# Optimization experiments

Hardware: AMD Instinct MI355X
Metric: run time of the kernel (lower is better)

Reference implementation:

```python
import jax, jax.numpy as jnp
import numpy as np
import math

B, N, D, H = 4, 2048, 1024, 16
HD = D // H  # head dim = 64


def setup_inputs() -> dict:
    key = jax.random.key(0)
    ks = jax.random.split(key, 5)
    x = jax.random.normal(ks[0], (B, N, D), dtype=jnp.float32)
    # per-head kqv Linear: weight (3*HD, D), bias (3*HD), stacked over heads
    Wkqv = jax.random.normal(ks[1], (H, 3 * HD, D), dtype=jnp.float32) / math.sqrt(D)
    bkqv = jax.random.normal(ks[2], (H, 3 * HD), dtype=jnp.float32) * 0.02
    # output projection Linear(D, D)
    Wproj = jax.random.normal(ks[3], (D, D), dtype=jnp.float32) / math.sqrt(D)
    bproj = jax.random.normal(ks[4], (D,), dtype=jnp.float32) * 0.02
    return {"x": x, "Wkqv": Wkqv, "bkqv": bkqv, "Wproj": Wproj, "bproj": bproj}


def reference(x, Wkqv, bkqv, Wproj, bproj):
    # per-head linear: y = x @ W.T + b  -> [B, H, N, 3*HD]
    kqv = jnp.einsum('bnd,hed->bhne', x, Wkqv) + bkqv[None, :, None, :]
    k, q, v = jnp.split(kqv, 3, axis=-1)  # each [B, H, N, HD]
    # scores = q @ k^T / sqrt(HD)   (attention_scores(k, q) -> q @ k.T)
    scores = jnp.einsum('bhqd,bhkd->bhqk', q, k) / math.sqrt(HD)
    causal = jnp.tril(jnp.ones((N, N), dtype=bool))
    scores = jnp.where(causal[None, None], scores, -jnp.inf)
    att = jax.nn.softmax(scores, axis=-1)
    out = jnp.einsum('bhqk,bhkd->bhqd', att, v)  # [B, H, N, HD]
    # concat heads: [B, N, H*HD]
    sa = out.transpose(0, 2, 1, 3).reshape(B, N, D)
    # dropout is identity in eval mode; final projection
    return sa @ Wproj.T + bproj
```

## Files before the change

kernel.cpp:

```cpp
#include <hip/hip_runtime.h>
#include <hip/hip_bf16.h>


#define NSEQ 2048
#define NHEAD 16
#define DMODEL 1024
#define SCALE2 0.18033688011112042f

typedef __attribute__((ext_vector_type(8))) short v8s;
typedef __attribute__((ext_vector_type(4))) float v4f;

__device__ __forceinline__ float bf2f(unsigned short u) {
    union { unsigned int i; float f; } v;
    v.i = ((unsigned int)u) << 16;
    return v.f;
}
__device__ __forceinline__ unsigned short f2bf(float f) {
    unsigned int x = __float_as_uint(f);
    return (unsigned short)((x + 0x7fffu + ((x >> 16) & 1u)) >> 16);
}
__device__ __forceinline__ unsigned short f2bf_rh(float f) {
    return (unsigned short)((__float_as_uint(f) + 0x8000u) >> 16);
}
__device__ __forceinline__ float fast_exp2(float x) {
#if __has_builtin(__builtin_amdgcn_exp2f)
    return __builtin_amdgcn_exp2f(x);
#else
    return __expf(x * 0.69314718056f);
#endif
}
__device__ __forceinline__ void gld_lds16(const unsigned short* g, unsigned short* l) {
    __builtin_amdgcn_global_load_lds(
        (const __attribute__((address_space(1))) void*)g,
        (__attribute__((address_space(3))) void*)l, 16, 0, 0);
}

__global__ __launch_bounds__(256) void cvt_bf16(
    const float* __restrict__ x, const float* __restrict__ wk, const float* __restrict__ wp,
    unsigned short* __restrict__ xb, unsigned short* __restrict__ wkb,
    unsigned short* __restrict__ wpb)
{
    const int i = blockIdx.x * 256 + threadIdx.x;
    const float* s; unsigned short* d; int o;
    if (i < 2097152)      { s = x;  d = xb;  o = i; }
    else if (i < 2883584) {
        s = wk; d = wkb;
        const int oi  = i - 2097152;
        const int row = oi >> 8, cq = oi & 255;
        const int h   = row / 192;
        const int rem = row - h * 192;
        const int cls = rem >> 6, e = rem & 63;
        float4 f = ((const float4*)s)[oi];
        ushort4 u;
        u.x = f2bf(f.x); u.y = f2bf(f.y); u.z = f2bf(f.z); u.w = f2bf(f.w);
        ((ushort4*)d)[(((cls << 10) + (h << 6) + e) << 8) + cq] = u;
        return;
    }
    else                  { s = wp; d = wpb; o = i - 2883584; }
    float4 f = ((const float4*)s)[o];
    ushort4 u;
    u.x = f2bf(f.x); u.y = f2bf(f.y); u.z = f2bf(f.z); u.w = f2bf(f.w);
    ((ushort4*)d)[o] = u;
}

template <int EPI>
__global__ __launch_bounds__(256, 3) void gemm_lds(
    const unsigned short* __restrict__ A, const unsigned short* __restrict__ B,
    const float* __restrict__ bias,
    float* __restrict__ Cf,
    unsigned short* __restrict__ Kb, unsigned short* __restrict__ Qb,
    unsigned short* __restrict__ VTb,
    int M, int Nc, int K)
{
    __shared__ __align__(16) unsigned short Al[3][4096];
    __shared__ __align__(16) unsigned short Bl[3][4096];

    const int t = threadIdx.x, wave = t >> 6, lane = t & 63;
    const int wm = wave >> 1, wn = wave & 1;

    const int lin = blockIdx.y * gridDim.x + blockIdx.x;
    const int xcd = lin & 7, pos = lin >> 3;
    const int by  = (xcd << 3) + (pos & 7);
    const int bx  = pos >> 3;
    const int m0 = by * 128, n0 = bx * 128;
    const int quad = lane >> 4, c = lane & 15;

    const int g0 = wave * 2, g1 = wave * 2 + 1;
    const int r15 = lane & 15, kg = (lane >> 4) & 3;
    const unsigned short* sA0 = A + (size_t)(m0 + g0 * 16 + r15) * K + kg * 8;
    const unsigned short* sA1 = A + (size_t)(m0 + g1 * 16 + r15) * K + kg * 8;
    const unsigned short* sB0 = B + (size_t)(n0 + g0 * 16 + r15) * K + kg * 8;
    const unsigned short* sB1 = B + (size_t)(n0 + g1 * 16 + r15) * K + kg * 8;

    v4f acc[4][4];
#pragma unroll
    for (int i = 0; i < 4; ++i)
#pragma unroll
        for (int j = 0; j < 4; ++j) acc[i][j] = (v4f){0.f, 0.f, 0.f, 0.f};

    const int fbase = (quad * 16 + c) * 8;
    const int nt = K >> 5;

    auto stage = [&](int b, int tt) {
        const int o = tt << 5;
        unsigned short* la = &Al[b][0];
        unsigned short* lb = &Bl[b][0];
        gld_lds16(sA0 + o, la + g0 * 512);
        gld_lds16(sA1 + o, la + g1 * 512);
        gld_lds16(sB0 + o, lb + g0 * 512);
        gld_lds16(sB1 + o, lb + g1 * 512);
    };

    stage(0, 0);
    stage(1, 1);
    asm volatile("s_waitcnt vmcnt(4)" ::: "memory");
    __builtin_amdgcn_s_barrier();

    int cur = 0;
    for (int tt = 0; tt < nt; ++tt) {
        const int nxt = (cur == 2) ? 0 : cur + 1;
        const int b2  = (nxt == 2) ? 0 : nxt + 1;
        const bool pf = (tt + 2 < nt);
        if (pf) stage(b2, tt + 2);

        v8s af[4], bfr[4];
#pragma unroll
        for (int ms = 0; ms < 4; ++ms)
            af[ms] = *(const v8s*)&Al[cur][(wm * 4 + ms) * 512 + fbase];
#pragma unroll
        for (int ns = 0; ns < 4; ++ns)
            bfr[ns] = *(const v8s*)&Bl[cur][(wn * 4 + ns) * 512 + fbase];
#pragma unroll
        for (int ms = 0; ms < 4; ++ms)
#pragma unroll
            for (int ns = 0; ns < 4; ++ns)
                acc[ms][ns] = __builtin_amdgcn_mfma_f32_16x16x32_bf16(
                    af[ms], bfr[ns], acc[ms][ns], 0, 0, 0);

        if (pf) { asm volatile("s_waitcnt vmcnt(4)" ::: "memory"); }
        else    { asm volatile("s_waitcnt vmcnt(0)" ::: "memory"); }
        __builtin_amdgcn_s_barrier();
        cur = nxt;
    }

#pragma unroll
    for (int ms = 0; ms < 4; ++ms) {
        const int row0 = m0 + wm * 64 + ms * 16 + quad * 4;
#pragma unroll
        for (int ns = 0; ns < 4; ++ns) {
            const int colbase = n0 + wn * 64 + ns * 16;
            float bn, scl = 1.f;
            if (EPI == 2) {
                bn = bias[colbase + c];
            } else {
                const int cls = colbase >> 10;
                const int wi  = colbase & 1023;
                const int h   = wi >> 6, e0 = wi & 63;
                bn = bias[h * 192 + cls * 64 + e0 + c];
                if (cls == 1) scl = SCALE2;
            }
            float v0 = (acc[ms][ns][0] + bn) * scl;
            float v1 = (acc[ms][ns][1] + bn) * scl;
            float v2 = (acc[ms][ns][2] + bn) * scl;
            float v3 = (acc[ms][ns][3] + bn) * scl;
            if (EPI == 2) {
                float* pc = Cf + (size_t)row0 * Nc + colbase + c;
                pc[0] = v0; pc[(size_t)Nc] = v1;
                pc[(size_t)2 * Nc] = v2; pc[(size_t)3 * Nc] = v3;
            } else {
                const int cls = colbase >> 10;
                const int wi  = colbase & 1023;
                const int h   = wi >> 6, e = (wi & 63) + c;
                const int bb  = row0 >> 11, tok0 = row0 & 2047;
                const int bhh = bb * 16 + h;
                if (cls == 2) {
                    ushort4 pk;
                    pk.x = f2bf(v0); pk.y = f2bf(v1); pk.z = f2bf(v2); pk.w = f2bf(v3);
                    *(ushort4*)(VTb + ((size_t)bhh * 64 + e) * 2048 + tok0) = pk;
                } else {
                    unsigned short* dst = (cls == 0) ? Kb : Qb;
                    const size_t base = ((size_t)bhh * 2048 + tok0) * 64 + e;
                    dst[base]       = f2bf(v0);
                    dst[base + 64]  = f2bf(v1);
                    dst[base + 128] = f2bf(v2);
                    dst[base + 192] = f2bf(v3);
                }
            }
        }
    }
}

template <bool A_BF16, int EPI>
__global__ __launch_bounds__(256) void gemm_mfma(
    const void* __restrict__ Av, const float* __restrict__ B,
    const float* __restrict__ bias,
    float* __restrict__ Cf,
    unsigned short* __restrict__ Kb, unsigned short* __restrict__ Qb,
    unsigned short* __restrict__ VTb,
    int M, int Nc, int K)
{
    __shared__ __align__(16) unsigned short Al[512 * 8];
    __shared__ __align__(16) unsigned short Bl[512 * 8];

    const int t = threadIdx.x;
    const int wave = t >> 6, lane = t & 63;
    const int wm = wave >> 1, wn = wave & 1;
    const int m0 = blockIdx.y * 128, n0 = blockIdx.x * 128;
    const int quad = lane >> 4, c = lane & 15;

    const int srow = t >> 1, skh = t & 1;
    const int sslot = (srow >> 4) * 64 + (skh * 2) * 16 + (srow & 15);

    v4f acc[4][4];
#pragma unroll
    for (int i = 0; i < 4; ++i)
#pragma unroll
        for (int j = 0; j < 4; ++j) acc[i][j] = (v4f){0.f, 0.f, 0.f, 0.f};

    const unsigned short* pa_u = (const unsigned short*)Av + (size_t)(m0 + srow) * K + skh * 16;
    const float*          pa_f = (const float*)Av          + (size_t)(m0 + srow) * K + skh * 16;
    const float*          pb   = B                          + (size_t)(n0 + srow) * K + skh * 16;

    const int fbase = (quad * 16 + c) * 8;

    for (int k0 = 0; k0 < K; k0 += 32) {
        unsigned short a16[16], b16[16];
        if (A_BF16) {
            uint4 r0 = *(const uint4*)(pa_u + k0);
            uint4 r1 = *(const uint4*)(pa_u + k0 + 8);
            *(uint4*)&a16[0] = r0; *(uint4*)&a16[8] = r1;
        } else {
            float4 f0 = *(const float4*)(pa_f + k0);
            float4 f1 = *(const float4*)(pa_f + k0 + 4);
            float4 f2 = *(const float4*)(pa_f + k0 + 8);
            float4 f3 = *(const float4*)(pa_f + k0 + 12);
            a16[0] = f2bf_rh(f0.x); a16[1] = f2bf_rh(f0.y); a16[2] = f2bf_rh(f0.z); a16[3] = f2bf_rh(f0.w);
            a16[4] = f2bf_rh(f1.x); a16[5] = f2bf_rh(f1.y); a16[6] = f2bf_rh(f1.z); a16[7] = f2bf_rh(f1.w);
            a16[8] = f2bf_rh(f2.x); a16[9] = f2bf_rh(f2.y); a16[10] = f2bf_rh(f2.z); a16[11] = f2bf_rh(f2.w);
            a16[12] = f2bf_rh(f3.x); a16[13] = f2bf_rh(f3.y); a16[14] = f2bf_rh(f3.z); a16[15] = f2bf_rh(f3.w);
        }
        {
            float4 g0 = *(const float4*)(pb + k0);
            float4 g1 = *(const float4*)(pb + k0 + 4);
            float4 g2 = *(const float4*)(pb + k0 + 8);
            float4 g3 = *(const float4*)(pb + k0 + 12);
            b16[0] = f2bf_rh(g0.x); b16[1] = f2bf_rh(g0.y); b16[2] = f2bf_rh(g0.z); b16[3] = f2bf_rh(g0.w);
            b16[4] = f2bf_rh(g1.x); b16[5] = f2bf_rh(g1.y); b16[6] = f2bf_rh(g1.z); b16[7] = f2bf_rh(g1.w);
            b16[8] = f2bf_rh(g2.x); b16[9] = f2bf_rh(g2.y); b16[10] = f2bf_rh(g2.z); b16[11] = f2bf_rh(g2.w);
            b16[12] = f2bf_rh(g3.x); b16[13] = f2bf_rh(g3.y); b16[14] = f2bf_rh(g3.z); b16[15] = f2bf_rh(g3.w);
        }
        __syncthreads();
        *(uint4*)&Al[sslot * 8]        = *(uint4*)&a16[0];
        *(uint4*)&Al[(sslot + 16) * 8] = *(uint4*)&a16[8];
        *(uint4*)&Bl[sslot * 8]        = *(uint4*)&b16[0];
        *(uint4*)&Bl[(sslot + 16) * 8] = *(uint4*)&b16[8];
        __syncthreads();

        v8s af[4], bf[4];
#pragma unroll
        for (int ms = 0; ms < 4; ++ms)
            af[ms] = *(const v8s*)&Al[(wm * 4 + ms) * 512 + fbase];
#pragma unroll
        for (int ns = 0; ns < 4; ++ns)
            bf[ns] = *(const v8s*)&Bl[(wn * 4 + ns) * 512 + fbase];
#pragma unroll
        for (int ms = 0; ms < 4; ++ms)
#pragma unroll
            for (int ns = 0; ns < 4; ++ns)
                acc[ms][ns] = __builtin_amdgcn_mfma_f32_16x16x32_bf16(
                    af[ms], bf[ns], acc[ms][ns], 0, 0, 0);
    }

#pragma unroll
    for (int ms = 0; ms < 4; ++ms) {
        const int row0 = m0 + wm * 64 + ms * 16 + quad * 4;
#pragma unroll
        for (int ns = 0; ns < 4; ++ns) {
            const int colbase = n0 + wn * 64 + ns * 16;
            float bn = (EPI == 2) ? bias[colbase + c] : bias[colbase + c];
            float v0 = acc[ms][ns][0] + bn;
            float v1 = acc[ms][ns][1] + bn;
            float v2 = acc[ms][ns][2] + bn;
            float v3 = acc[ms][ns][3] + bn;
            if (EPI == 2) {
                float* pc = Cf + (size_t)row0 * Nc + colbase + c;
                pc[0] = v0; pc[(size_t)Nc] = v1;
                pc[(size_t)2 * Nc] = v2; pc[(size_t)3 * Nc] = v3;
            } else {
                const int hh = colbase / 192;
                const int eb = colbase - hh * 192;
                const int bb = row0 >> 11, tok0 = row0 & 2047;
                const int bhh = bb * 16 + hh;
                if (eb >= 128) {
                    ushort4 pk;
                    pk.x = f2bf(v0); pk.y = f2bf(v1); pk.z = f2bf(v2); pk.w = f2bf(v3);
                    *(ushort4*)(VTb + ((size_t)bhh * 64 + (eb - 128) + c) * 2048 + tok0) = pk;
                } else {
                    const bool isq = (eb >= 64);
                    const float s = isq ? SCALE2 : 1.f;
                    unsigned short* dst = isq ? Qb : Kb;
                    const int e = (isq ? eb - 64 : eb) + c;
                    const size_t base = ((size_t)bhh * 2048 + tok0) * 64 + e;
                    dst[base]       = f2bf(v0 * s);
                    dst[base + 64]  = f2bf(v1 * s);
                    dst[base + 128] = f2bf(v2 * s);
                    dst[base + 192] = f2bf(v3 * s);
                }
            }
        }
    }
}

#define ATTS 72

__global__ __launch_bounds__(256, 2) void attn_mfma(
    const unsigned short* __restrict__ Kbuf,
    const unsigned short* __restrict__ Qbuf,
    const unsigned short* __restrict__ VT,
    unsigned short* __restrict__ sa)
{
    __shared__ __align__(16) unsigned short Ps[4][64 * ATTS];

    const int t = threadIdx.x, w = t >> 6, lane = t & 63;
    const int quad = lane >> 4, c = lane & 15;
    const int bh = blockIdx.x & 63, bq = blockIdx.x >> 6;
    const int b = bh >> 4, hh = bh & 15;
    const int qt = (w == 0) ? bq : (w == 1) ? (15 - bq) : (w == 2) ? (16 + bq) : (31 - bq);
    const int qw = qt * 64;
    const size_t gbase = (size_t)bh * (2048 * 64);

    const int rs  = c & 3;
    const int rc0 = (quad ^ rs) * 8, rc1 = 32 + rc0;
    unsigned short* PsW = &Ps[w][0];

    v8s qf[4][2];
#pragma unroll
    for (int qs = 0; qs < 4; ++qs) {
        const unsigned short* qp = Qbuf + gbase + (size_t)(qw + qs * 16 + c) * 64 + quad * 8;
        qf[qs][0] = *(const v8s*)qp;
        qf[qs][1] = *(const v8s*)(qp + 32);
    }
    v4f oacc[4][4], lacc[4];
#pragma unroll
    for (int qs = 0; qs < 4; ++qs) {
        lacc[qs] = (v4f){0.f, 0.f, 0.f, 0.f};
#pragma unroll
        for (int dn = 0; dn < 4; ++dn) oacc[qs][dn] = (v4f){0.f, 0.f, 0.f, 0.f};
    }
    const short oneb = (short)0x3F80;
    const v8s ones = {oneb, oneb, oneb, oneb, oneb, oneb, oneb, oneb};

    const int nkt = qt + 1;
    for (int kt = 0; kt < nkt; ++kt) {
        const int kbase = kt * 64;
        const bool diag = (kt == nkt - 1);
#pragma unroll
        for (int kn = 0; kn < 4; ++kn) {
            const unsigned short* kp =
                Kbuf + gbase + (size_t)(kbase + kn * 16 + c) * 64 + quad * 8;
            v8s kf0 = *(const v8s*)kp;
            v8s kf1 = *(const v8s*)(kp + 32);
#pragma unroll
            for (int qs = 0; qs < 4; ++qs) {
                v4f s = (v4f){0.f, 0.f, 0.f, 0.f};
                s = __builtin_amdgcn_mfma_f32_16x16x32_bf16(qf[qs][0], kf0, s, 0, 0, 0);
                s = __builtin_amdgcn_mfma_f32_16x16x32_bf16(qf[qs][1], kf1, s, 0, 0, 0);
                if (diag) {
#pragma unroll
                    for (int r = 0; r < 4; ++r)
                        if (kn * 16 + c > qs * 16 + quad * 4 + r) s[r] = -1e30f;
                }
#pragma unroll
                for (int r = 0; r < 4; ++r) {
                    const float p = fast_exp2(s[r]);
                    PsW[(qs * 16 + quad * 4 + r) * ATTS +
                        (((2 * kn + (c >> 3)) ^ r) * 8) + (c & 7)] = f2bf_rh(p);
                }
            }
        }
        v8s pa[4][2];
#pragma unroll
        for (int qs = 0; qs < 4; ++qs) {
            pa[qs][0] = *(const v8s*)&PsW[(qs * 16 + c) * ATTS + rc0];
            pa[qs][1] = *(const v8s*)&PsW[(qs * 16 + c) * ATTS + rc1];
        }
#pragma unroll
        for (int dn = 0; dn < 4; ++dn) {
            const unsigned short* vp =
                VT + gbase + (size_t)(dn * 16 + c) * 2048 + kbase + quad * 8;
            v8s vf0 = *(const v8s*)vp;
            v8s vf1 = *(const v8s*)(vp + 32);
#pragma unroll
            for (int qs = 0; qs < 4; ++qs) {
                oacc[qs][dn] = __builtin_amdgcn_mfma_f32_16x16x32_bf16(pa[qs][0], vf0, oacc[qs][dn], 0, 0, 0);
                oacc[qs][dn] = __builtin_amdgcn_mfma_f32_16x16x32_bf16(pa[qs][1], vf1, oacc[qs][dn], 0, 0, 0);
            }
        }
#pragma unroll
        for (int qs = 0; qs < 4; ++qs) {
            lacc[qs] = __builtin_amdgcn_mfma_f32_16x16x32_bf16(pa[qs][0], ones, lacc[qs], 0, 0, 0);
            lacc[qs] = __builtin_amdgcn_mfma_f32_16x16x32_bf16(pa[qs][1], ones, lacc[qs], 0, 0, 0);
        }
    }

#pragma unroll
    for (int qs = 0; qs < 4; ++qs) {
        float inv[4];
#pragma unroll
        for (int r = 0; r < 4; ++r) inv[r] = 1.f / lacc[qs][r];
        const size_t obase =
            ((size_t)(b * 2048 + qw + qs * 16 + quad * 4)) * DMODEL + hh * 64;
#pragma unroll
        for (int dn = 0; dn < 4; ++dn)
#pragma unroll
            for (int r = 0; r < 4; ++r)
                sa[obase + (size_t)r * DMODEL + dn * 16 + c] = f2bf(oacc[qs][dn][r] * inv[r]);
    }
}

extern "C" void kernel_launch(void* const* d_in, const int* in_sizes, int n_in,
                              void* d_out, int out_size, void* d_ws, size_t ws_size,
                              hipStream_t stream) {
    const float* x     = (const float*)d_in[0];
    const float* Wkqv  = (const float*)d_in[1];
    const float* bkqv  = (const float*)d_in[2];
    const float* Wproj = (const float*)d_in[3];
    const float* bproj = (const float*)d_in[4];
    float* out = (float*)d_out;

    unsigned short* Kb = (unsigned short*)d_ws;
    unsigned short* Qb = Kb + (size_t)8388608;
    unsigned short* VT = Qb + (size_t)8388608;
    unsigned short* sa = VT + (size_t)8388608;

    const bool fast = ws_size >= 75497472ull;
    if (fast) {
        unsigned short* xb  = sa;
        unsigned short* wkb = (unsigned short*)d_ws + (size_t)33554432;
        unsigned short* wpb = wkb + (size_t)3145728;
        cvt_bf16<<<12288, 256, 0, stream>>>(x, Wkqv, Wproj, xb, wkb, wpb);
        gemm_lds<1><<<dim3(24, 64), 256, 0, stream>>>(
            xb, wkb, bkqv, nullptr, Kb, Qb, VT, 8192, 3072, 1024);
        attn_mfma<<<512, 256, 0, stream>>>(Kb, Qb, VT, sa);
        gemm_lds<2><<<dim3(8, 64), 256, 0, stream>>>(
            sa, wpb, bproj, out, nullptr, nullptr, nullptr, 8192, 1024, 1024);
    } else {
        gemm_mfma<false, 1><<<dim3(24, 64), 256, 0, stream>>>(
            x, Wkqv, bkqv, nullptr, Kb, Qb, VT, 8192, 3072, 1024);
        attn_mfma<<<512, 256, 0, stream>>>(Kb, Qb, VT, sa);
        gemm_mfma<true, 2><<<dim3(8, 64), 256, 0, stream>>>(
            sa, Wproj, bproj, out, nullptr, nullptr, nullptr, 8192, 1024, 1024);
    }
}
```

Measured before the change: 318.2 us.

## Enlarge GEMM tiles to 256x256 with 8 waves and 4-stage ping-pong pipeline

The LDS-staged bf16 GEMM moves from 128x128 tiles with 4 waves and 3 stages to 256x256 tiles with 8 waves and 4 stages. Each wave now computes 128x64, and each k-step is split into two MFMA halves with A/B prefetches interleaved between barriers and s_setprio raised around the MFMA blocks. The intent is more data reuse per global load and better overlap of loads with math. In exchange it uses 128KB of LDS and more accumulator registers, and the grid shrinks to 384 and 128 blocks, which may underfill the GPU for the projection GEMM.

```diff
diff --git a/kernel.cpp b/kernel.cpp
--- a/kernel.cpp
+++ b/kernel.cpp
@@ -64,7 +64,7 @@
 }
 
 template <int EPI>
-__global__ __launch_bounds__(256, 3) void gemm_lds(
+__global__ __launch_bounds__(512, 2) void gemm_lds(
     const unsigned short* __restrict__ A, const unsigned short* __restrict__ B,
     const float* __restrict__ bias,
     float* __restrict__ Cf,
@@ -72,17 +72,17 @@
     unsigned short* __restrict__ VTb,
     int M, int Nc, int K)
 {
-    __shared__ __align__(16) unsigned short Al[3][4096];
-    __shared__ __align__(16) unsigned short Bl[3][4096];
+    __shared__ __align__(16) unsigned short Al[4][8192];
+    __shared__ __align__(16) unsigned short Bl[4][8192];
 
     const int t = threadIdx.x, wave = t >> 6, lane = t & 63;
-    const int wm = wave >> 1, wn = wave & 1;
+    const int wm = wave >> 2, wn = wave & 3;
 
     const int lin = blockIdx.y * gridDim.x + blockIdx.x;
     const int xcd = lin & 7, pos = lin >> 3;
-    const int by  = (xcd << 3) + (pos & 7);
-    const int bx  = pos >> 3;
-    const int m0 = by * 128, n0 = bx * 128;
+    const int by  = (xcd << 2) + (pos & 3);
+    const int bx  = pos >> 2;
+    const int m0 = by * 256, n0 = bx * 256;
     const int quad = lane >> 4, c = lane & 15;
 
     const int g0 = wave * 2, g1 = wave * 2 + 1;
@@ -92,60 +92,83 @@
     const unsigned short* sB0 = B + (size_t)(n0 + g0 * 16 + r15) * K + kg * 8;
     const unsigned short* sB1 = B + (size_t)(n0 + g1 * 16 + r15) * K + kg * 8;
 
-    v4f acc[4][4];
-#pragma unroll
-    for (int i = 0; i < 4; ++i)
+    v4f acc[8][4];
+#pragma unroll
+    for (int i = 0; i < 8; ++i)
 #pragma unroll
         for (int j = 0; j < 4; ++j) acc[i][j] = (v4f){0.f, 0.f, 0.f, 0.f};
 
     const int fbase = (quad * 16 + c) * 8;
     const int nt = K >> 5;
 
-    auto stage = [&](int b, int tt) {
+    auto stageA = [&](int sl, int tt) {
         const int o = tt << 5;
-        unsigned short* la = &Al[b][0];
-        unsigned short* lb = &Bl[b][0];
+        unsigned short* la = &Al[sl][0];
         gld_lds16(sA0 + o, la + g0 * 512);
         gld_lds16(sA1 + o, la + g1 * 512);
+    };
+    auto stageB = [&](int sl, int tt) {
+        const int o = tt << 5;
+        unsigned short* lb = &Bl[sl][0];
         gld_lds16(sB0 + o, lb + g0 * 512);
         gld_lds16(sB1 + o, lb + g1 * 512);
     };
 
-    stage(0, 0);
-    stage(1, 1);
-    asm volatile("s_waitcnt vmcnt(4)" ::: "memory");
+    stageA(0, 0); stageB(0, 0);
+    stageA(1, 1); stageB(1, 1);
+    stageA(2, 2); stageB(2, 2);
+    asm volatile("s_waitcnt vmcnt(8)" ::: "memory");
     __builtin_amdgcn_s_barrier();
 
-    int cur = 0;
     for (int tt = 0; tt < nt; ++tt) {
-        const int nxt = (cur == 2) ? 0 : cur + 1;
-        const int b2  = (nxt == 2) ? 0 : nxt + 1;
-        const bool pf = (tt + 2 < nt);
-        if (pf) stage(b2, tt + 2);
-
-        v8s af[4], bfr[4];
-#pragma unroll
-        for (int ms = 0; ms < 4; ++ms)
-            af[ms] = *(const v8s*)&Al[cur][(wm * 4 + ms) * 512 + fbase];
+        const int sl  = tt & 3;
+        const int sl3 = (tt + 3) & 3;
+        const bool pf = (tt + 3 < nt);
+
+        v8s bfr[4], af[4];
 #pragma unroll
         for (int ns = 0; ns < 4; ++ns)
-            bfr[ns] = *(const v8s*)&Bl[cur][(wn * 4 + ns) * 512 + fbase];
+            bfr[ns] = *(const v8s*)&Bl[sl][(wn * 4 + ns) * 512 + fbase];
+#pragma unroll
+        for (int ms = 0; ms < 4; ++ms)
+            af[ms] = *(const v8s*)&Al[sl][(wm * 8 + ms) * 512 + fbase];
+        if (pf) stageA(sl3, tt + 3);
+        __builtin_amdgcn_s_barrier();
+        asm volatile("s_waitcnt lgkmcnt(0)" ::: "memory");
+        __builtin_amdgcn_s_setprio(1);
 #pragma unroll
         for (int ms = 0; ms < 4; ++ms)
 #pragma unroll
             for (int ns = 0; ns < 4; ++ns)
                 acc[ms][ns] = __builtin_amdgcn_mfma_f32_16x16x32_bf16(
                     af[ms], bfr[ns], acc[ms][ns], 0, 0, 0);
-
-        if (pf) { asm volatile("s_waitcnt vmcnt(4)" ::: "memory"); }
-        else    { asm volatile("s_waitcnt vmcnt(0)" ::: "memory"); }
+        __builtin_amdgcn_s_setprio(0);
         __builtin_amdgcn_s_barrier();
-        cur = nxt;
-    }
-
-#pragma unroll
-    for (int ms = 0; ms < 4; ++ms) {
-        const int row0 = m0 + wm * 64 + ms * 16 + quad * 4;
+
+        v8s af2[4];
+#pragma unroll
+        for (int ms = 0; ms < 4; ++ms)
+            af2[ms] = *(const v8s*)&Al[sl][(wm * 8 + 4 + ms) * 512 + fbase];
+        if (pf) stageB(sl3, tt + 3);
+        __builtin_amdgcn_s_barrier();
+        asm volatile("s_waitcnt lgkmcnt(0)" ::: "memory");
+        __builtin_amdgcn_s_setprio(1);
+#pragma unroll
+        for (int ms = 0; ms < 4; ++ms)
+#pragma unroll
+            for (int ns = 0; ns < 4; ++ns)
+                acc[4 + ms][ns] = __builtin_amdgcn_mfma_f32_16x16x32_bf16(
+                    af2[ms], bfr[ns], acc[4 + ms][ns], 0, 0, 0);
+        __builtin_amdgcn_s_setprio(0);
+        if (pf)                   { asm volatile("s_waitcnt vmcnt(8)" ::: "memory"); }
+        else if (tt + 2 < nt)     { asm volatile("s_waitcnt vmcnt(4)" ::: "memory"); }
+        else                      { asm volatile("s_waitcnt vmcnt(0)" ::: "memory"); }
+        __builtin_amdgcn_s_barrier();
+    }
+
+#pragma unroll
+    for (int ms = 0; ms < 8; ++ms) {
+        const int row0 = m0 + wm * 128 + ms * 16 + quad * 4;
 #pragma unroll
         for (int ns = 0; ns < 4; ++ns) {
             const int colbase = n0 + wn * 64 + ns * 16;
@@ -439,10 +462,10 @@
         unsigned short* wkb = (unsigned short*)d_ws + (size_t)33554432;
         unsigned short* wpb = wkb + (size_t)3145728;
         cvt_bf16<<<12288, 256, 0, stream>>>(x, Wkqv, Wproj, xb, wkb, wpb);
-        gemm_lds<1><<<dim3(24, 64), 256, 0, stream>>>(
+        gemm_lds<1><<<dim3(12, 32), 512, 0, stream>>>(
             xb, wkb, bkqv, nullptr, Kb, Qb, VT, 8192, 3072, 1024);
         attn_mfma<<<512, 256, 0, stream>>>(Kb, Qb, VT, sa);
-        gemm_lds<2><<<dim3(8, 64), 256, 0, stream>>>(
+        gemm_lds<2><<<dim3(4, 32), 512, 0, stream>>>(
             sa, wpb, bproj, out, nullptr, nullptr, nullptr, 8192, 1024, 1024);
     } else {
         gemm_mfma<false, 1><<<dim3(24, 64), 256, 0, stream>>>(
```

Measured after the change: 312.5 us. Within noise of the previous version (-1.8%).
